# Kernel tuning notes

Hardware: AMD Instinct MI355X
Metric: run time of the kernel (lower is better)

Reference implementation:

```python
import jax, jax.numpy as jnp
import numpy as np
import math

B, S, H, NH, NKV, HD = 1, 2048, 4096, 32, 8, 128
ROPE_THETA = 10000.0


def setup_inputs() -> dict:
    key = jax.random.key(0)
    ks = jax.random.split(key, 16)
    hidden_states = jax.random.normal(ks[0], (B, S, H), jnp.float32) * 0.02
    Wq = jax.random.normal(ks[1], (NH * HD, H), jnp.float32) * 0.02
    Wk = jax.random.normal(ks[2], (NKV * HD, H), jnp.float32) * 0.02
    Wv = jax.random.normal(ks[3], (NKV * HD, H), jnp.float32) * 0.02
    Wo = jax.random.normal(ks[4], (H, NH * HD), jnp.float32) * 0.02
    # RoPE cos/sin, HF Llama convention: emb = concat(freqs, freqs)
    inv_freq = 1.0 / (ROPE_THETA ** (jnp.arange(0, HD, 2, dtype=jnp.float32) / HD))
    pos = jnp.arange(S, dtype=jnp.float32)
    freqs = pos[:, None] * inv_freq[None, :]              # [S, HD/2]
    emb = jnp.concatenate([freqs, freqs], axis=-1)        # [S, HD]
    cos = jnp.cos(emb)[None]                              # [1, S, HD]
    sin = jnp.sin(emb)[None]
    # additive causal mask [B, 1, S, S]
    causal = jnp.tril(jnp.ones((S, S), dtype=bool))
    attention_mask = jnp.where(causal, 0.0, -1e9).astype(jnp.float32)[None, None]
    # reorder permutations (as written by GPTQ act-order reordering)
    perm = lambda k, n: jax.random.permutation(k, n).astype(jnp.int32)
    return {
        'hidden_states': hidden_states, 'Wq': Wq, 'Wk': Wk, 'Wv': Wv, 'Wo': Wo,
        'cos': cos, 'sin': sin, 'attention_mask': attention_mask,
        'q_order_col': perm(ks[5], H), 'q_order_row': perm(ks[6], NH * HD),
        'k_order_col': perm(ks[7], H), 'k_order_row': perm(ks[8], NKV * HD),
        'v_order_col': perm(ks[9], H), 'v_order_row': perm(ks[10], NKV * HD),
        'o_order_col': perm(ks[11], NH * HD), 'o_order_row': perm(ks[12], H),
    }


def _rotate_half(x):
    x1, x2 = jnp.split(x, 2, axis=-1)
    return jnp.concatenate([-x2, x1], axis=-1)


def reference(hidden_states, Wq, Wk, Wv, Wo, cos, sin, attention_mask,
              q_order_col, q_order_row, k_order_col, k_order_row,
              v_order_col, v_order_row, o_order_col, o_order_row):
    bsz, q_len, _ = hidden_states.shape
    # permuted projections: gather cols of input, GEMM, gather rows of output
    q = hidden_states[:, :, q_order_col] @ Wq.T
    q = q[:, :, q_order_row]
    k = hidden_states[:, :, k_order_col] @ Wk.T
    k = k[:, :, k_order_row]
    v = hidden_states[:, :, v_order_col] @ Wv.T
    v = v[:, :, v_order_row]
    q = q.reshape(bsz, q_len, NH, HD).transpose(0, 2, 1, 3)   # [B,NH,S,HD]
    k = k.reshape(bsz, q_len, NKV, HD).transpose(0, 2, 1, 3)  # [B,NKV,S,HD]
    v = v.reshape(bsz, q_len, NKV, HD).transpose(0, 2, 1, 3)
    # RoPE
    c = cos[:, None, :, :]  # [1,1,S,HD]
    s = sin[:, None, :, :]
    q = q * c + _rotate_half(q) * s
    k = k * c + _rotate_half(k) * s
    # repeat_kv for GQA
    rep = NH // NKV
    k = jnp.repeat(k, rep, axis=1)  # [B,NH,S,HD]
    v = jnp.repeat(v, rep, axis=1)
    # eager attention: full score matrix, fp32 softmax
    scores = jnp.einsum('bhqd,bhkd->bhqk', q, k) / math.sqrt(HD)
    scores = scores + attention_mask
    probs = jax.nn.softmax(scores.astype(jnp.float32), axis=-1).astype(q.dtype)
    # dropout p=0.0 (eval) -> identity
    attn = jnp.einsum('bhqk,bhkd->bhqd', probs, v)
    attn = attn.transpose(0, 2, 1, 3).reshape(bsz, q_len, NH * HD)
    out = attn[:, :, o_order_col] @ Wo.T
    out = out[:, :, o_order_row]
    return out
```

## Files before the change

kernel.cpp:

```cpp
#include <hip/hip_runtime.h>

typedef unsigned short u16;
typedef unsigned char u8;
typedef __bf16 bf16x8 __attribute__((ext_vector_type(8)));
typedef float f32x4 __attribute__((ext_vector_type(4)));
typedef int i32x4 __attribute__((ext_vector_type(4)));
typedef int i32x8 __attribute__((ext_vector_type(8)));

__device__ __forceinline__ u16 f2bf(float f) {
    unsigned u = __float_as_uint(f);
    unsigned r = (u + 0x7fffu + ((u >> 16) & 1u)) >> 16;
    return (u16)r;
}
__device__ __forceinline__ float bf2f(u16 h) {
    return __uint_as_float(((unsigned)h) << 16);
}
__device__ __forceinline__ unsigned pack_bf2(float lo, float hi) {
    unsigned a = __float_as_uint(hi) + 0x8000u;
    unsigned b = __float_as_uint(lo) + 0x8000u;
    return __builtin_amdgcn_perm(a, b, 0x07060302u);
}
__device__ __forceinline__ unsigned pack_fp8x4(float a, float b, float c, float d) {
    unsigned w = __builtin_amdgcn_cvt_pk_fp8_f32(a, b, 0, false);
    w = __builtin_amdgcn_cvt_pk_fp8_f32(c, d, w, true);
    return w;
}
__device__ __forceinline__ void async_copy16(const void* g, void* l) {
    __builtin_amdgcn_global_load_lds((__attribute__((address_space(1))) void*)(void*)g,
                                     (__attribute__((address_space(3))) void*)l, 16, 0, 0);
}

#define FP8_SCALE 64.0f
#define FP8_UNSCALE (1.0f / 4096.0f)


__global__ void inv4_k(const int* __restrict__ q, const int* __restrict__ k,
                       const int* __restrict__ v, const int* __restrict__ o,
                       int* __restrict__ invq, int* __restrict__ invk,
                       int* __restrict__ invv, int* __restrict__ invo) {
    int i = blockIdx.x * 256 + threadIdx.x;
    int a = i >> 12, j = i & 4095;
    const int* p = a == 0 ? q : a == 1 ? k : a == 2 ? v : o;
    int* inv = a == 0 ? invq : a == 1 ? invk : a == 2 ? invv : invo;
    inv[p[j]] = j;
}

__global__ __launch_bounds__(256) void permw4_k(
    const float* __restrict__ Wq, const float* __restrict__ Wk,
    const float* __restrict__ Wv, const float* __restrict__ Wo,
    const int* __restrict__ qor, const int* __restrict__ kor,
    const int* __restrict__ vor, const int* __restrict__ oor,
    const int* __restrict__ invq, const int* __restrict__ invk,
    const int* __restrict__ invv, const int* __restrict__ invo,
    u8* __restrict__ Wqkf8, u16* __restrict__ Wvp, u16* __restrict__ Wop) {
    __shared__ float rowbuf[4096];
    int j = blockIdx.x;
    const float* W; const int* rp; const int* inv; int row; int f8;
    u8* out8 = nullptr; u16* out16 = nullptr;
    if (j < 4096)      { W = Wq; rp = qor; inv = invq; row = j;        out8 = Wqkf8 + (size_t)j * 4096; f8 = 1; }
    else if (j < 5120) { W = Wk; rp = kor; inv = invk; row = j - 4096; out8 = Wqkf8 + (size_t)j * 4096; f8 = 1; }
    else if (j < 6144) { W = Wv; rp = vor; inv = invv; row = j - 5120; out16 = Wvp + (size_t)(j - 5120) * 4096; f8 = 0; }
    else               { W = Wo; rp = oor; inv = invo; row = j - 6144; out16 = Wop + (size_t)(j - 6144) * 4096; f8 = 0; }
    const float4* wr4 = (const float4*)(W + (size_t)rp[row] * 4096);
#pragma unroll
    for (int t = 0; t < 4; t++)
        ((float4*)rowbuf)[threadIdx.x + t * 256] = wr4[threadIdx.x + t * 256];
    __syncthreads();
    if (f8) {
        int t = threadIdx.x;
        const int4* inv4p = (const int4*)inv;
        float v[16];
#pragma unroll
        for (int u = 0; u < 4; u++) {
            int4 ix = inv4p[t * 4 + u];
            v[4 * u + 0] = rowbuf[ix.x] * FP8_SCALE;
            v[4 * u + 1] = rowbuf[ix.y] * FP8_SCALE;
            v[4 * u + 2] = rowbuf[ix.z] * FP8_SCALE;
            v[4 * u + 3] = rowbuf[ix.w] * FP8_SCALE;
        }
        uint4 wv;
        wv.x = pack_fp8x4(v[0], v[1], v[2], v[3]);
        wv.y = pack_fp8x4(v[4], v[5], v[6], v[7]);
        wv.z = pack_fp8x4(v[8], v[9], v[10], v[11]);
        wv.w = pack_fp8x4(v[12], v[13], v[14], v[15]);
        int tb = (t & ~7) | ((t & 7) ^ (j & 7));
        ((uint4*)out8)[tb] = wv;
    } else {
        unsigned* o32 = (unsigned*)out16;
        const int2* inv2 = (const int2*)inv;
#pragma unroll
        for (int t = 0; t < 8; t++) {
            int c = threadIdx.x + t * 256;
            int2 ij = inv2[c];
            o32[c] = pack_bf2(rowbuf[ij.x], rowbuf[ij.y]);
        }
    }
}

__global__ __launch_bounds__(256) void cvt_k(const float* __restrict__ x,
                                             u16* __restrict__ Xb,
                                             u8* __restrict__ Xf8) {
    int row = blockIdx.x;
    int t = threadIdx.x;
    const float4* src = (const float4*)(x + (size_t)row * 4096);
    float v[16];
#pragma unroll
    for (int u = 0; u < 4; u++) {
        float4 a = src[t * 4 + u];
        v[4 * u + 0] = a.x; v[4 * u + 1] = a.y; v[4 * u + 2] = a.z; v[4 * u + 3] = a.w;
    }
    uint4 b0, b1;
    b0.x = pack_bf2(v[0], v[1]);  b0.y = pack_bf2(v[2], v[3]);
    b0.z = pack_bf2(v[4], v[5]);  b0.w = pack_bf2(v[6], v[7]);
    b1.x = pack_bf2(v[8], v[9]);  b1.y = pack_bf2(v[10], v[11]);
    b1.z = pack_bf2(v[12], v[13]); b1.w = pack_bf2(v[14], v[15]);
    uint4* ob = (uint4*)(Xb + (size_t)row * 4096);
    ob[t * 2] = b0;
    ob[t * 2 + 1] = b1;
    uint4 w8;
    w8.x = pack_fp8x4(v[0] * FP8_SCALE, v[1] * FP8_SCALE, v[2] * FP8_SCALE, v[3] * FP8_SCALE);
    w8.y = pack_fp8x4(v[4] * FP8_SCALE, v[5] * FP8_SCALE, v[6] * FP8_SCALE, v[7] * FP8_SCALE);
    w8.z = pack_fp8x4(v[8] * FP8_SCALE, v[9] * FP8_SCALE, v[10] * FP8_SCALE, v[11] * FP8_SCALE);
    w8.w = pack_fp8x4(v[12] * FP8_SCALE, v[13] * FP8_SCALE, v[14] * FP8_SCALE, v[15] * FP8_SCALE);
    int tb = (t & ~7) | ((t & 7) ^ (row & 7));
    ((uint4*)(Xf8 + (size_t)row * 4096))[tb] = w8;
}

__global__ __launch_bounds__(256) void rope_tr_k(u16* __restrict__ X,
                                                 const float* __restrict__ cosv,
                                                 const float* __restrict__ sinv,
                                                 const float* __restrict__ Vpart,
                                                 u16* __restrict__ Vt) {
    __shared__ u16 t[64][65];
    if (blockIdx.x < 20480) {
        int tt = blockIdx.x * 256 + threadIdx.x;
        int d = tt & 63;
        int rest = tt >> 6;
        int head = rest % 40;
        int s = rest / 40;
        size_t base = (size_t)s * 6144 + head * 128 + d;
        float x1 = bf2f(X[base]), x2 = bf2f(X[base + 64]);
        float c1 = cosv[s * 128 + d], s1 = sinv[s * 128 + d];
        float c2 = cosv[s * 128 + d + 64], s2 = sinv[s * 128 + d + 64];
        float sc = head < 32 ? 0.08838834764831845f : 1.0f;
        X[base]      = f2bf((x1 * c1 - x2 * s1) * sc);
        X[base + 64] = f2bf((x2 * c2 + x1 * s2) * sc);
    } else {
        int bx = blockIdx.x - 20480;
        int s0 = (bx & 31) * 64, c0 = (bx >> 5) * 64;
        int x = threadIdx.x & 63, y4 = threadIdx.x >> 6;
        const float* Vp0 = Vpart;
        const float* Vp1 = Vpart + (size_t)2048 * 1024;
        for (int i = 0; i < 16; i++) {
            int r = y4 * 16 + i;
            size_t idx = (size_t)(s0 + r) * 1024 + c0 + x;
            t[r][x] = f2bf(Vp0[idx] + Vp1[idx]);
        }
        __syncthreads();
        for (int i = 0; i < 16; i++) {
            int r = y4 * 16 + i;
            int xk = 4 * (x & 15) + (x >> 4);
            Vt[(size_t)(c0 + r) * 2048 + s0 + xk] = t[x][r];
        }
    }
}


__global__ __launch_bounds__(256) void gemm_qkv_k(const u8* __restrict__ Xf8,
                                                  const u16* __restrict__ Xb,
                                                  const u8* __restrict__ Wqk,
                                                  const u16* __restrict__ Wv,
                                                  u16* __restrict__ QKV,
                                                  float* __restrict__ Vpart) {
    __shared__ u8 lds[32768];
    const int tid = threadIdx.x;
    const int w = tid >> 6, lane = tid & 63;
    const int quad = lane >> 4, l16 = lane & 15;
    const int bm0 = blockIdx.y * 128;
    const int wm = (w >> 1) * 64, wn = (w & 1) * 64;
    if (blockIdx.x < 40) {
        const int bn0 = blockIdx.x * 128;
        u8* ldsA = lds;
        u8* ldsB = lds + 16384;
        const u8* Ag = Xf8 + (size_t)(bm0 + w * 32 + (lane >> 3)) * 4096 + (lane & 7) * 16;
        const u8* Bg = Wqk + (size_t)(bn0 + w * 32 + (lane >> 3)) * 4096 + (lane & 7) * 16;
        u8* la = ldsA + w * 32 * 128;
        u8* lb = ldsB + w * 32 * 128;
        const int swz = l16 & 7;
        f32x4 acc[4][4] = {};
        for (int k0 = 0; k0 < 4096; k0 += 128) {
#pragma unroll
            for (int t = 0; t < 4; t++) async_copy16(Ag + (size_t)t * 8 * 4096 + k0, la + t * 1024);
#pragma unroll
            for (int t = 0; t < 4; t++) async_copy16(Bg + (size_t)t * 8 * 4096 + k0, lb + t * 1024);
            __syncthreads();
            i32x8 af[4], bf[4];
#pragma unroll
            for (int i = 0; i < 4; i++) {
                int r = wm + i * 16 + l16;
                union { i32x8 v8; i32x4 v4[2]; } u;
                u.v4[0] = *(const i32x4*)&ldsA[r * 128 + ((quad * 2) ^ swz) * 16];
                u.v4[1] = *(const i32x4*)&ldsA[r * 128 + ((quad * 2 + 1) ^ swz) * 16];
                af[i] = u.v8;
            }
#pragma unroll
            for (int j = 0; j < 4; j++) {
                int r = wn + j * 16 + l16;
                union { i32x8 v8; i32x4 v4[2]; } u;
                u.v4[0] = *(const i32x4*)&ldsB[r * 128 + ((quad * 2) ^ swz) * 16];
                u.v4[1] = *(const i32x4*)&ldsB[r * 128 + ((quad * 2 + 1) ^ swz) * 16];
                bf[j] = u.v8;
            }
#pragma unroll
            for (int i = 0; i < 4; i++)
#pragma unroll
                for (int j = 0; j < 4; j++)
                    acc[i][j] = __builtin_amdgcn_mfma_scale_f32_16x16x128_f8f6f4(
                        af[i], bf[j], acc[i][j], 0, 0,
                        0, 0x7F7F7F7F, 0, 0x7F7F7F7F);
            __syncthreads();
        }
#pragma unroll
        for (int i = 0; i < 4; i++) {
            const int row = bm0 + wm + i * 16 + quad * 4;
#pragma unroll
            for (int j = 0; j < 4; j++) {
                const int col = bn0 + wn + j * 16 + l16;
#pragma unroll
                for (int r = 0; r < 4; r++)
                    QKV[(size_t)(row + r) * 6144 + col] = f2bf(acc[i][j][r] * FP8_UNSCALE);
            }
        }
    } else {
        const int vx = blockIdx.x - 40;
        const int bn0 = (vx & 7) * 128;
        const int kslice = vx >> 3;
        const int kb = kslice * 2048;
        u16* lds_a0 = (u16*)lds;
        u16* lds_a1 = (u16*)(lds + 8192);
        u16* lds_b0 = (u16*)(lds + 16384);
        u16* lds_b1 = (u16*)(lds + 24576);
        const int r0 = w * 16 + (lane >> 2);
        const int c0 = (lane & 3) * 8;
        const u16* Ag = Xb + (size_t)(bm0 + r0) * 4096 + kb + c0;
        const u16* Bg = Wv + (size_t)(bn0 + r0) * 4096 + kb + c0;
        f32x4 acc[4][4] = {};
        for (int k0 = 0; k0 < 2048; k0 += 64) {
            async_copy16(Ag + k0,                         lds_a0 + w * 512);
            async_copy16(Ag + (size_t)64 * 4096 + k0,     lds_a0 + (w + 4) * 512);
            async_copy16(Ag + k0 + 32,                    lds_a1 + w * 512);
            async_copy16(Ag + (size_t)64 * 4096 + k0 + 32, lds_a1 + (w + 4) * 512);
            async_copy16(Bg + k0,                         lds_b0 + w * 512);
            async_copy16(Bg + (size_t)64 * 4096 + k0,     lds_b0 + (w + 4) * 512);
            async_copy16(Bg + k0 + 32,                    lds_b1 + w * 512);
            async_copy16(Bg + (size_t)64 * 4096 + k0 + 32, lds_b1 + (w + 4) * 512);
            __syncthreads();
#pragma unroll
            for (int kk = 0; kk < 2; kk++) {
                const u16* la = kk ? lds_a1 : lds_a0;
                const u16* lb = kk ? lds_b1 : lds_b0;
                bf16x8 af[4], bfv[4];
#pragma unroll
                for (int i = 0; i < 4; i++)
                    af[i] = *(const bf16x8*)&la[(wm + i * 16 + l16) * 32 + quad * 8];
#pragma unroll
                for (int j = 0; j < 4; j++)
                    bfv[j] = *(const bf16x8*)&lb[(wn + j * 16 + l16) * 32 + quad * 8];
#pragma unroll
                for (int i = 0; i < 4; i++)
#pragma unroll
                    for (int j = 0; j < 4; j++)
                        acc[i][j] = __builtin_amdgcn_mfma_f32_16x16x32_bf16(af[i], bfv[j], acc[i][j], 0, 0, 0);
            }
            __syncthreads();
        }
        float* Vp = Vpart + (size_t)kslice * 2048 * 1024;
#pragma unroll
        for (int i = 0; i < 4; i++) {
            const int row = bm0 + wm + i * 16 + quad * 4;
#pragma unroll
            for (int j = 0; j < 4; j++) {
                const int col = bn0 + wn + j * 16 + l16;
#pragma unroll
                for (int r = 0; r < 4; r++)
                    Vp[(size_t)(row + r) * 1024 + col] = acc[i][j][r];
            }
        }
    }
}


__global__ __launch_bounds__(256) void gemm_bt_k(const u16* __restrict__ A,
                                                 const u16* __restrict__ B,
                                                 float* __restrict__ C,
                                                 int M, int N, int K) {
    __shared__ u16 lds_a[128 * 32];
    __shared__ u16 lds_b[128 * 32];
    const int tid = threadIdx.x;
    const int w = tid >> 6, lane = tid & 63;
    const int quad = lane >> 4, l16 = lane & 15;
    const int bm0 = blockIdx.y * 128, bn0 = blockIdx.x * 128;
    const int wm = (w >> 1) * 64, wn = (w & 1) * 64;
    const int r0 = w * 16 + (lane >> 2);
    const int c0 = (lane & 3) * 8;
    const u16* Ag = A + (size_t)(bm0 + r0) * K + c0;
    const u16* Bg = B + (size_t)(bn0 + r0) * K + c0;
    u16* la0 = &lds_a[w * 512];
    u16* la1 = &lds_a[(w + 4) * 512];
    u16* lb0 = &lds_b[w * 512];
    u16* lb1 = &lds_b[(w + 4) * 512];

    f32x4 acc[4][4] = {};
    for (int k0 = 0; k0 < K; k0 += 32) {
        async_copy16(Ag + k0, la0);
        async_copy16(Ag + (size_t)64 * K + k0, la1);
        async_copy16(Bg + k0, lb0);
        async_copy16(Bg + (size_t)64 * K + k0, lb1);
        __syncthreads();
        bf16x8 af[4], bf[4];
#pragma unroll
        for (int i = 0; i < 4; i++)
            af[i] = *(const bf16x8*)&lds_a[(wm + i * 16 + l16) * 32 + quad * 8];
#pragma unroll
        for (int j = 0; j < 4; j++)
            bf[j] = *(const bf16x8*)&lds_b[(wn + j * 16 + l16) * 32 + quad * 8];
#pragma unroll
        for (int i = 0; i < 4; i++)
#pragma unroll
            for (int j = 0; j < 4; j++)
                acc[i][j] = __builtin_amdgcn_mfma_f32_16x16x32_bf16(af[i], bf[j], acc[i][j], 0, 0, 0);
        __syncthreads();
    }
#pragma unroll
    for (int i = 0; i < 4; i++) {
        const int row = bm0 + wm + i * 16 + quad * 4;
#pragma unroll
        for (int j = 0; j < 4; j++) {
            const int col = bn0 + wn + j * 16 + l16;
#pragma unroll
            for (int r = 0; r < 4; r++)
                C[(size_t)(row + r) * N + col] = acc[i][j][r];
        }
    }
}


__global__ __launch_bounds__(256) void attn_k(const u16* __restrict__ Qb,
                                              const u16* __restrict__ Kb,
                                              const u16* __restrict__ Vt,
                                              u16* __restrict__ Ob,
                                              int qstride, int kstride) {
    __shared__ u16 ldsK[4 * 64 * 32];
    __shared__ u16 ldsV[2 * 128 * 32];
    __shared__ u16 ldsP[4][32 * 72];
    const int h = blockIdx.x;
    const int qt = (int)gridDim.y - 1 - (int)blockIdx.y;
    const int kvh = h >> 2;
    const int tid = threadIdx.x;
    const int w = tid >> 6, lane = tid & 63;
    const int quad = lane >> 4, l16 = lane & 15;
    const int q0 = qt * 128;
    const int wrow = q0 + w * 32;

    bf16x8 qf[2][4];
#pragma unroll
    for (int mi = 0; mi < 2; mi++)
#pragma unroll
        for (int kk = 0; kk < 4; kk++)
            qf[mi][kk] = *(const bf16x8*)&Qb[(size_t)(wrow + mi * 16 + l16) * qstride +
                                             h * 128 + kk * 32 + quad * 8];

    const u16* kp[4]; const u16* vp[4];
    u16* ldk[4]; u16* ldv[4];
#pragma unroll
    for (int t = 0; t < 4; t++) {
        int wl = w + t * 4;
        int kk = wl >> 2, part = wl & 3;
        kp[t] = Kb + (size_t)(part * 16 + (lane >> 2)) * kstride + kvh * 128 + kk * 32 + (lane & 3) * 8;
        int ks2 = wl >> 3, p2 = wl & 7;
        vp[t] = Vt + (size_t)(kvh * 128 + p2 * 16 + (lane >> 2)) * 2048 + ks2 * 32 + (lane & 3) * 8;
        ldk[t] = ldsK + wl * 512;
        ldv[t] = ldsV + wl * 512;
    }

    f32x4 acc_o[2][8] = {};
    float lrow[2][4] = {};

    const int nk = 2 * (qt + 1);
    for (int kn = 0; kn < nk; kn++) {
        const int g0 = kn * 64;
#pragma unroll
        for (int t = 0; t < 4; t++) async_copy16(kp[t], ldk[t]);
#pragma unroll
        for (int t = 0; t < 4; t++) async_copy16(vp[t], ldv[t]);
#pragma unroll
        for (int t = 0; t < 4; t++) { kp[t] += (size_t)64 * kstride; vp[t] += 64; }
        __syncthreads();

        if (g0 <= wrow + 31) {
            f32x4 accs[2][4] = {};
#pragma unroll
            for (int kk = 0; kk < 4; kk++) {
                bf16x8 bfrag[4];
#pragma unroll
                for (int ni = 0; ni < 4; ni++)
                    bfrag[ni] = *(const bf16x8*)&ldsK[kk * 2048 + (ni * 16 + l16) * 32 + quad * 8];
#pragma unroll
                for (int mi = 0; mi < 2; mi++)
#pragma unroll
                    for (int ni = 0; ni < 4; ni++)
                        accs[mi][ni] = __builtin_amdgcn_mfma_f32_16x16x32_bf16(
                            qf[mi][kk], bfrag[ni], accs[mi][ni], 0, 0, 0);
            }
            const bool diag = (g0 + 63 > wrow);
            int kidx[4];
#pragma unroll
            for (int ni = 0; ni < 4; ni++) kidx[ni] = g0 + ni * 16 + l16;
#pragma unroll
            for (int mi = 0; mi < 2; mi++) {
#pragma unroll
                for (int r = 0; r < 4; r++) {
                    const int qrow = wrow + mi * 16 + quad * 4 + r;
                    float p[4];
#pragma unroll
                    for (int ni = 0; ni < 4; ni++) {
                        float s = accs[mi][ni][r];
                        if (diag && (kidx[ni] > qrow)) s = -1e30f;
                        p[ni] = __expf(s);
                    }
                    lrow[mi][r] += (p[0] + p[1]) + (p[2] + p[3]);
                    uint2 pk;
                    pk.x = pack_bf2(p[0], p[1]);
                    pk.y = pack_bf2(p[2], p[3]);
                    *(uint2*)&ldsP[w][(mi * 16 + quad * 4 + r) * 72 + l16 * 4] = pk;
                }
            }
#pragma unroll
            for (int ks = 0; ks < 2; ks++) {
                bf16x8 pa[2];
#pragma unroll
                for (int mi = 0; mi < 2; mi++)
                    pa[mi] = *(const bf16x8*)&ldsP[w][(mi * 16 + l16) * 72 + ks * 32 + quad * 8];
#pragma unroll
                for (int oj = 0; oj < 8; oj++) {
                    bf16x8 vb = *(const bf16x8*)&ldsV[ks * 4096 + (oj * 16 + l16) * 32 + quad * 8];
#pragma unroll
                    for (int mi = 0; mi < 2; mi++)
                        acc_o[mi][oj] = __builtin_amdgcn_mfma_f32_16x16x32_bf16(
                            pa[mi], vb, acc_o[mi][oj], 0, 0, 0);
                }
            }
        }
        __syncthreads();
    }
#pragma unroll
    for (int mi = 0; mi < 2; mi++)
#pragma unroll
        for (int r = 0; r < 4; r++) {
            float l = lrow[mi][r];
            l += __shfl_xor(l, 1);
            l += __shfl_xor(l, 2);
            l += __shfl_xor(l, 4);
            l += __shfl_xor(l, 8);
            const float inv = 1.0f / l;
            const int qrow = wrow + mi * 16 + quad * 4 + r;
#pragma unroll
            for (int oj = 0; oj < 8; oj++)
                Ob[(size_t)qrow * 4096 + h * 128 + oj * 16 + l16] =
                    f2bf(acc_o[mi][oj][r] * inv);
        }
}


extern "C" void kernel_launch(void* const* d_in, const int* in_sizes, int n_in,
                              void* d_out, int out_size, void* d_ws, size_t ws_size,
                              hipStream_t stream) {
    (void)in_sizes; (void)n_in; (void)out_size; (void)ws_size;
    const float* hidden = (const float*)d_in[0];
    const float* Wq = (const float*)d_in[1];
    const float* Wk = (const float*)d_in[2];
    const float* Wv = (const float*)d_in[3];
    const float* Wo = (const float*)d_in[4];
    const float* cosv = (const float*)d_in[5];
    const float* sinv = (const float*)d_in[6];
    const int* qoc = (const int*)d_in[8];
    const int* qor = (const int*)d_in[9];
    const int* koc = (const int*)d_in[10];
    const int* kor = (const int*)d_in[11];
    const int* voc = (const int*)d_in[12];
    const int* vor = (const int*)d_in[13];
    const int* ooc = (const int*)d_in[14];
    const int* oor = (const int*)d_in[15];

    char* ws = (char*)d_ws;
    size_t off = 0;
    int* invq = (int*)(ws + off); off += 16384;
    int* invk = (int*)(ws + off); off += 16384;
    int* invv = (int*)(ws + off); off += 16384;
    int* invo = (int*)(ws + off); off += 16384;
    u8*  Wqkf8 = (u8*)(ws + off);  off += (size_t)5120 * 4096;
    u16* Wvp   = (u16*)(ws + off); off += (size_t)1024 * 4096 * 2;
    u16* Wop   = (u16*)(ws + off); off += (size_t)4096 * 4096 * 2;
    u16* Xb    = (u16*)(ws + off); off += (size_t)2048 * 4096 * 2;
    u8*  Xf8   = (u8*)(ws + off);  off += (size_t)2048 * 4096;
    u16* QKVb  = (u16*)(ws + off); off += (size_t)2048 * 6144 * 2;
    u16* Vtb   = (u16*)(ws + off); off += (size_t)1024 * 2048 * 2;
    float* Vpart = (float*)(ws + off); off += (size_t)2 * 2048 * 1024 * 4;
    u16* Attb  = Xb;

    inv4_k<<<64, 256, 0, stream>>>(qoc, koc, voc, ooc, invq, invk, invv, invo);
    permw4_k<<<10240, 256, 0, stream>>>(Wq, Wk, Wv, Wo, qor, kor, vor, oor,
                                        invq, invk, invv, invo, Wqkf8, Wvp, Wop);
    cvt_k<<<2048, 256, 0, stream>>>(hidden, Xb, Xf8);

    gemm_qkv_k<<<dim3(56, 16), 256, 0, stream>>>(Xf8, Xb, Wqkf8, Wvp, QKVb, Vpart);

    rope_tr_k<<<20992, 256, 0, stream>>>(QKVb, cosv, sinv, Vpart, Vtb);

    attn_k<<<dim3(32, 16), 256, 0, stream>>>(QKVb, QKVb + 4096, Vtb, Attb, 6144, 6144);

    gemm_bt_k<<<dim3(32, 16), 256, 0, stream>>>(Attb, Wop, (float*)d_out, 2048, 4096, 4096);
}
```

Baseline: 530.4 us.

## Split-K the output projection GEMM with 64-wide K steps and reduce partials

The output projection GEMM now splits K into two halves, launching 1024 blocks instead of 512 so more CUs get work. Each K iteration loads two 32-wide slabs into LDS, halving the number of barriers per unit of work. Each half writes fp32 partials into a reused workspace region, and a separate reduce kernel sums them into the output. The cost is extra traffic writing and rereading 2x32MB of fp32 partials, plus one more launch.

Measured after the change: 524.9 us. About the same (-1.0%).

```diff
diff --git a/kernel.cpp b/kernel.cpp
--- a/kernel.cpp
+++ b/kernel.cpp
@@ -290,47 +290,57 @@
 }
 
 
-__global__ __launch_bounds__(256) void gemm_bt_k(const u16* __restrict__ A,
-                                                 const u16* __restrict__ B,
-                                                 float* __restrict__ C,
-                                                 int M, int N, int K) {
-    __shared__ u16 lds_a[128 * 32];
-    __shared__ u16 lds_b[128 * 32];
+__global__ __launch_bounds__(256) void gemm_o_k(const u16* __restrict__ A,
+                                                const u16* __restrict__ B,
+                                                float* __restrict__ Opart) {
+    __shared__ u16 lds[16384];
+    u16* lds_a0 = lds;
+    u16* lds_a1 = lds + 4096;
+    u16* lds_b0 = lds + 8192;
+    u16* lds_b1 = lds + 12288;
     const int tid = threadIdx.x;
     const int w = tid >> 6, lane = tid & 63;
     const int quad = lane >> 4, l16 = lane & 15;
-    const int bm0 = blockIdx.y * 128, bn0 = blockIdx.x * 128;
+    const int bm0 = blockIdx.y * 128;
+    const int bn0 = (blockIdx.x & 31) * 128;
+    const int kslice = blockIdx.x >> 5;
+    const int kb = kslice * 2048;
     const int wm = (w >> 1) * 64, wn = (w & 1) * 64;
     const int r0 = w * 16 + (lane >> 2);
     const int c0 = (lane & 3) * 8;
-    const u16* Ag = A + (size_t)(bm0 + r0) * K + c0;
-    const u16* Bg = B + (size_t)(bn0 + r0) * K + c0;
-    u16* la0 = &lds_a[w * 512];
-    u16* la1 = &lds_a[(w + 4) * 512];
-    u16* lb0 = &lds_b[w * 512];
-    u16* lb1 = &lds_b[(w + 4) * 512];
-
+    const u16* Ag = A + (size_t)(bm0 + r0) * 4096 + kb + c0;
+    const u16* Bg = B + (size_t)(bn0 + r0) * 4096 + kb + c0;
     f32x4 acc[4][4] = {};
-    for (int k0 = 0; k0 < K; k0 += 32) {
-        async_copy16(Ag + k0, la0);
-        async_copy16(Ag + (size_t)64 * K + k0, la1);
-        async_copy16(Bg + k0, lb0);
-        async_copy16(Bg + (size_t)64 * K + k0, lb1);
+    for (int k0 = 0; k0 < 2048; k0 += 64) {
+        async_copy16(Ag + k0,                          lds_a0 + w * 512);
+        async_copy16(Ag + (size_t)64 * 4096 + k0,      lds_a0 + (w + 4) * 512);
+        async_copy16(Ag + k0 + 32,                     lds_a1 + w * 512);
+        async_copy16(Ag + (size_t)64 * 4096 + k0 + 32, lds_a1 + (w + 4) * 512);
+        async_copy16(Bg + k0,                          lds_b0 + w * 512);
+        async_copy16(Bg + (size_t)64 * 4096 + k0,      lds_b0 + (w + 4) * 512);
+        async_copy16(Bg + k0 + 32,                     lds_b1 + w * 512);
+        async_copy16(Bg + (size_t)64 * 4096 + k0 + 32, lds_b1 + (w + 4) * 512);
         __syncthreads();
-        bf16x8 af[4], bf[4];
-#pragma unroll
-        for (int i = 0; i < 4; i++)
-            af[i] = *(const bf16x8*)&lds_a[(wm + i * 16 + l16) * 32 + quad * 8];
-#pragma unroll
-        for (int j = 0; j < 4; j++)
-            bf[j] = *(const bf16x8*)&lds_b[(wn + j * 16 + l16) * 32 + quad * 8];
-#pragma unroll
-        for (int i = 0; i < 4; i++)
+#pragma unroll
+        for (int kk = 0; kk < 2; kk++) {
+            const u16* la = kk ? lds_a1 : lds_a0;
+            const u16* lb = kk ? lds_b1 : lds_b0;
+            bf16x8 af[4], bfv[4];
+#pragma unroll
+            for (int i = 0; i < 4; i++)
+                af[i] = *(const bf16x8*)&la[(wm + i * 16 + l16) * 32 + quad * 8];
 #pragma unroll
             for (int j = 0; j < 4; j++)
-                acc[i][j] = __builtin_amdgcn_mfma_f32_16x16x32_bf16(af[i], bf[j], acc[i][j], 0, 0, 0);
+                bfv[j] = *(const bf16x8*)&lb[(wn + j * 16 + l16) * 32 + quad * 8];
+#pragma unroll
+            for (int i = 0; i < 4; i++)
+#pragma unroll
+                for (int j = 0; j < 4; j++)
+                    acc[i][j] = __builtin_amdgcn_mfma_f32_16x16x32_bf16(af[i], bfv[j], acc[i][j], 0, 0, 0);
+        }
         __syncthreads();
     }
+    float* Op = Opart + (size_t)kslice * 2048 * 4096;
 #pragma unroll
     for (int i = 0; i < 4; i++) {
         const int row = bm0 + wm + i * 16 + quad * 4;
@@ -339,9 +349,18 @@
             const int col = bn0 + wn + j * 16 + l16;
 #pragma unroll
             for (int r = 0; r < 4; r++)
-                C[(size_t)(row + r) * N + col] = acc[i][j][r];
-        }
-    }
+                Op[(size_t)(row + r) * 4096 + col] = acc[i][j][r];
+        }
+    }
+}
+
+__global__ void reduce_k(const float* __restrict__ P, float* __restrict__ out) {
+    size_t i = (size_t)blockIdx.x * 256 + threadIdx.x;
+    float4 a = ((const float4*)P)[i];
+    float4 b = ((const float4*)(P + (size_t)2048 * 4096))[i];
+    float4 r;
+    r.x = a.x + b.x; r.y = a.y + b.y; r.z = a.z + b.z; r.w = a.w + b.w;
+    ((float4*)out)[i] = r;
 }
 
 
@@ -498,14 +517,16 @@
     int* invk = (int*)(ws + off); off += 16384;
     int* invv = (int*)(ws + off); off += 16384;
     int* invo = (int*)(ws + off); off += 16384;
+    u16* Wop   = (u16*)(ws + off); off += (size_t)4096 * 4096 * 2;
+    u16* Xb    = (u16*)(ws + off); off += (size_t)2048 * 4096 * 2;
+    size_t trans = off;
     u8*  Wqkf8 = (u8*)(ws + off);  off += (size_t)5120 * 4096;
     u16* Wvp   = (u16*)(ws + off); off += (size_t)1024 * 4096 * 2;
-    u16* Wop   = (u16*)(ws + off); off += (size_t)4096 * 4096 * 2;
-    u16* Xb    = (u16*)(ws + off); off += (size_t)2048 * 4096 * 2;
     u8*  Xf8   = (u8*)(ws + off);  off += (size_t)2048 * 4096;
     u16* QKVb  = (u16*)(ws + off); off += (size_t)2048 * 6144 * 2;
     u16* Vtb   = (u16*)(ws + off); off += (size_t)1024 * 2048 * 2;
     float* Vpart = (float*)(ws + off); off += (size_t)2 * 2048 * 1024 * 4;
+    float* Opart = (float*)(ws + trans);
     u16* Attb  = Xb;
 
     inv4_k<<<64, 256, 0, stream>>>(qoc, koc, voc, ooc, invq, invk, invv, invo);
@@ -519,5 +540,6 @@
 
     attn_k<<<dim3(32, 16), 256, 0, stream>>>(QKVb, QKVb + 4096, Vtb, Attb, 6144, 6144);
 
-    gemm_bt_k<<<dim3(32, 16), 256, 0, stream>>>(Attb, Wop, (float*)d_out, 2048, 4096, 4096);
-}
+    gemm_o_k<<<dim3(64, 16), 256, 0, stream>>>(Attb, Wop, Opart);
+    reduce_k<<<8192, 256, 0, stream>>>(Opart, (float*)d_out);
+}
```
